# Optimization experiments

Hardware: AMD Instinct MI355X
Metric: run time of the kernel (lower is better)

The kernel has to match this reference:

```python
import jax, jax.numpy as jnp
import numpy as np

E, TOP_K = 8, 2
NEG_SLOPE = 0.01  # nn.LeakyReLU default


def setup_inputs() -> dict:
    key = jax.random.key(0)
    ks = jax.random.split(key, 8)
    B, S, H, F, R = 2, 4096, 2048, 8192, 16
    s_h = 1.0 / np.sqrt(H)
    s_f = 1.0 / np.sqrt(F)
    s_r = 1.0 / np.sqrt(R)
    return {
        "x": jax.random.normal(ks[0], (B, S, H), jnp.float32),
        "gate_w": jax.random.normal(ks[1], (E, H), jnp.float32) * s_h,
        "w1_A": jax.random.normal(ks[2], (E, R, H), jnp.float32) * s_h,
        "w1_B": jax.random.normal(ks[3], (E, F, R), jnp.float32) * s_r,
        "w2_A": jax.random.normal(ks[4], (E, R, F), jnp.float32) * s_f,
        "w2_B": jax.random.normal(ks[5], (E, H, R), jnp.float32) * s_r,
        "w3_A": jax.random.normal(ks[6], (E, R, H), jnp.float32) * s_h,
        "w3_B": jax.random.normal(ks[7], (E, F, R), jnp.float32) * s_r,
    }


def reference(x, gate_w, w1_A, w1_B, w2_A, w2_B, w3_A, w3_B):
    B, S, H = x.shape
    xs = x.reshape(-1, H)  # [T,H]
    # router: softmax in fp32, top-k, renormalize (matches torch code)
    logits = xs @ gate_w.T  # [T,E]
    probs = jax.nn.softmax(logits.astype(jnp.float32), axis=-1)
    rw, sel = jax.lax.top_k(probs, TOP_K)  # [T,K]
    rw = rw / jnp.sum(rw, axis=-1, keepdims=True)
    rw = rw.astype(x.dtype)
    # per-token per-expert combine weight (0 if expert not selected) [T,E]
    w_te = jnp.sum(jax.nn.one_hot(sel, E, dtype=rw.dtype) * rw[..., None], axis=1)
    out = jnp.zeros_like(xs)
    for e in range(E):  # small fixed expert loop; avoids [E,T,F] blowup
        h1 = (xs @ w1_A[e].T) @ w1_B[e].T          # [T,F]
        h3 = (xs @ w3_A[e].T) @ w3_B[e].T          # [T,F]
        h = jnp.where(h1 >= 0, h1, NEG_SLOPE * h1) * h3
        y = (h @ w2_A[e].T) @ w2_B[e].T            # [T,H]
        out = out + y * w_te[:, e:e + 1]
    return out.reshape(B, S, H), rw
```

## Files before the change

kernel.cpp:

```cpp
#include <hip/hip_runtime.h>
#include <hip/hip_bf16.h>

typedef __attribute__((ext_vector_type(8))) short short8;
typedef __attribute__((ext_vector_type(4))) float f32x4;
typedef __hip_bfloat16 bf16;

static constexpr int T_TOK = 8192;
static constexpr int HD    = 2048;
static constexpr int FD    = 8192;
static constexpr int NE    = 8;

#define MFMA16(a,b,c) __builtin_amdgcn_mfma_f32_16x16x32_bf16((a),(b),(c),0,0,0)

__global__ __launch_bounds__(256) void k_convert(
    const float* __restrict__ w1A, const float* __restrict__ w1B,
    const float* __restrict__ w2A, const float* __restrict__ w2B,
    const float* __restrict__ w3A, const float* __restrict__ w3B,
    bf16* __restrict__ bw1a3, bf16* __restrict__ bw1b, bf16* __restrict__ bw3b,
    bf16* __restrict__ bw2apk, bf16* __restrict__ bw2b, int* __restrict__ cnt)
{
  int i = blockIdx.x * 256 + threadIdx.x;
  if (blockIdx.x == 0 && threadIdx.x < 16) cnt[threadIdx.x] = 0;
  bw1b[i] = __float2bfloat16(w1B[i]);
  bw3b[i] = __float2bfloat16(w3B[i]);
  {
    int f = i & (FD - 1); int er = i >> 13; int e = er >> 4; int r = er & 15;
    int ft = f >> 5; int fo = f & 31;
    int sub = fo >> 4; int lg = (fo >> 2) & 3; int j = sub * 4 + (fo & 3);
    int lane = lg * 16 + r;
    bw2apk[((e * 256 + ft) * 64 + lane) * 8 + j] = __float2bfloat16(w2A[i]);
  }
  if (i < 256 * HD) {
    int h = i & (HD - 1); int nn = i >> 11; int e = nn >> 5; int rr = nn & 31;
    float v = (rr < 16) ? w1A[(e * 16 + rr) * HD + h] : w3A[(e * 16 + (rr - 16)) * HD + h];
    bw1a3[e * 65536 + (h >> 5) * 1024 + rr * 32 + (h & 31)] = __float2bfloat16(v);
  }
  if (i < NE * HD * 16) bw2b[i] = __float2bfloat16(w2B[i]);
}

__global__ __launch_bounds__(512) void k_router(
    const float* __restrict__ x, const float* __restrict__ gw,
    float* __restrict__ rw_out, int* __restrict__ cnt,
    int* __restrict__ tok, float* __restrict__ wl, int* __restrict__ selT,
    bf16* __restrict__ bx, int use_bx)
{
  int tid = threadIdx.x;
  int j = tid >> 5;
  int r = tid & 31;
  int t = blockIdx.x * 16 + j;

  const float4* xr = reinterpret_cast<const float4*>(x + (size_t)t * HD);
  float p[8];
#pragma unroll
  for (int e = 0; e < 8; e++) p[e] = 0.f;
#pragma unroll 4
  for (int it = 0; it < 16; it++) {
    float4 xv = xr[it * 32 + r];
#pragma unroll
    for (int e = 0; e < 8; e++) {
      float4 gv = reinterpret_cast<const float4*>(gw + e * HD)[it * 32 + r];
      p[e] += xv.x * gv.x + xv.y * gv.y + xv.z * gv.z + xv.w * gv.w;
    }
    if (use_bx) {
      alignas(8) bf16 tb[4];
      tb[0] = __float2bfloat16(xv.x); tb[1] = __float2bfloat16(xv.y);
      tb[2] = __float2bfloat16(xv.z); tb[3] = __float2bfloat16(xv.w);
      *reinterpret_cast<uint2*>(bx + (size_t)t * HD + (it * 32 + r) * 4) =
          *reinterpret_cast<const uint2*>(tb);
    }
  }
#pragma unroll
  for (int e = 0; e < 8; e++) {
#pragma unroll
    for (int m = 1; m <= 16; m <<= 1) p[e] += __shfl_xor(p[e], m);
  }

  __shared__ int   se0[16], se1[16];
  __shared__ float sw0[16], sw1[16];
  if (r == 0) {
    float m = -1e30f;
#pragma unroll
    for (int e = 0; e < 8; e++) m = fmaxf(m, p[e]);
    float q[8];
#pragma unroll
    for (int e = 0; e < 8; e++) q[e] = __expf(p[e] - m);
    int i0 = 0; float b0 = q[0];
#pragma unroll
    for (int e = 1; e < 8; e++) if (q[e] > b0) { b0 = q[e]; i0 = e; }
    int i1 = -1; float b1 = -1.f;
#pragma unroll
    for (int e = 0; e < 8; e++) if (e != i0 && q[e] > b1) { b1 = q[e]; i1 = e; }
    float inv = 1.f / (b0 + b1);
    float r0 = b0 * inv, r1 = b1 * inv;
    rw_out[t * 2 + 0] = r0; rw_out[t * 2 + 1] = r1;
    selT[t] = i0 | (i1 << 8);
    se0[j] = i0; se1[j] = i1; sw0[j] = r0; sw1[j] = r1;
  }
  __syncthreads();
  if (tid < 16) {
    int ls = tid, e = ls >> 1, slot = ls & 1;
    int c = 0;
#pragma unroll
    for (int jj = 0; jj < 16; jj++)
      c += (slot == 0 ? (se0[jj] == e) : (se1[jj] == e)) ? 1 : 0;
    if (c > 0) {
      int base = atomicAdd(&cnt[ls], c);
      int k = 0;
#pragma unroll
      for (int jj = 0; jj < 16; jj++) {
        bool hit = (slot == 0 ? (se0[jj] == e) : (se1[jj] == e));
        if (hit) {
          tok[ls * T_TOK + base + k] = blockIdx.x * 16 + jj;
          wl [ls * T_TOK + base + k] = (slot == 0 ? sw0[jj] : sw1[jj]);
          k++;
        }
      }
    }
  }
}

#define LDW(FT, B1, B3, W2) { \
    int f0_ = w * 1024 + (FT) * 32; \
    _Pragma("unroll") \
    for (int sub = 0; sub < 2; sub++) { \
      int f_ = f0_ + sub * 16 + lm; \
      B1[sub] = *reinterpret_cast<const short8*>(w1e + f_ * 16 + r8); \
      B3[sub] = *reinterpret_cast<const short8*>(w3e + f_ * 16 + r8); \
    } \
    W2 = *reinterpret_cast<const short8*>(w2e + ((size_t)(f0_ >> 5) * 64 + l) * 8); }

#define CMP(B1, B3, W2) \
  _Pragma("unroll") \
  for (int m = 0; m < 2; m++) { \
    short8 hfrag; \
    _Pragma("unroll") \
    for (int sub = 0; sub < 2; sub++) { \
      f32x4 h1 = MFMA16(B1[sub], A1[m], zf); \
      f32x4 h3 = MFMA16(B3[sub], A3[m], zf); \
      _Pragma("unroll") \
      for (int i = 0; i < 4; i++) { \
        float a = h1[i]; \
        float hv = (a >= 0.f ? a : 0.01f * a) * h3[i]; \
        bf16 hb = __float2bfloat16(hv); \
        hfrag[sub * 4 + i] = *reinterpret_cast<short*>(&hb); \
      } \
    } \
    acc[m] = MFMA16(W2, hfrag, acc[m]); }

__global__ __launch_bounds__(512) void k_fused(
    const float* __restrict__ x, const bf16* __restrict__ bx, int use_bx,
    const bf16* __restrict__ bw1a3,
    const bf16* __restrict__ bw1b, const bf16* __restrict__ bw3b,
    const bf16* __restrict__ bw2apk,
    const int* __restrict__ cnt, const int* __restrict__ tok,
    const float* __restrict__ wl, bf16* __restrict__ accbf)
{
  int item = blockIdx.x;
  int ls = ((item & 7) << 1) | ((item >> 3) & 1);
  int pt = item >> 4;
  int n = cnt[ls]; int p0 = pt * 32;
  if (p0 >= n) return;
  int e = ls >> 1;
  int tid = threadIdx.x;
  int w = tid >> 6, l = tid & 63, lm = l & 15, lg = l >> 4;

  __shared__ int toks[32];
  __shared__ __align__(16) bf16 aT[32 * 40];
  __shared__ __align__(16) char uni[4352 * 4];
  float* part = reinterpret_cast<float*>(uni);
  float* red  = reinterpret_cast<float*>(uni);

  const f32x4 zf = {0.f, 0.f, 0.f, 0.f};
  const short8 ZS = {0, 0, 0, 0, 0, 0, 0, 0};

  if (tid < 32) {
    int pos = p0 + tid; if (pos > n - 1) pos = n - 1;
    toks[tid] = tok[ls * T_TOK + pos];
  }
  __syncthreads();

  {
    int tg = w >> 2, ks = w & 3;
    const bf16* be = bw1a3 + e * 65536 + ks * 16384 + lg * 8;
    f32x4 a0 = zf, a1 = zf, a2 = zf, a3 = zf;
    if (use_bx) {
      const bf16* xp = bx + (size_t)toks[tg * 16 + lm] * HD + ks * 512 + lg * 8;
#pragma unroll 4
      for (int k2 = 0; k2 < 8; k2++) {
        short8 af0 = *reinterpret_cast<const short8*>(xp + (2 * k2) * 32);
        short8 af1 = *reinterpret_cast<const short8*>(xp + (2 * k2 + 1) * 32);
        short8 b00 = *reinterpret_cast<const short8*>(be + (2 * k2) * 1024 + lm * 32);
        short8 b01 = *reinterpret_cast<const short8*>(be + (2 * k2) * 1024 + (lm + 16) * 32);
        short8 b10 = *reinterpret_cast<const short8*>(be + (2 * k2 + 1) * 1024 + lm * 32);
        short8 b11 = *reinterpret_cast<const short8*>(be + (2 * k2 + 1) * 1024 + (lm + 16) * 32);
        a0 = MFMA16(af0, b00, a0);
        a1 = MFMA16(af0, b01, a1);
        a2 = MFMA16(af1, b10, a2);
        a3 = MFMA16(af1, b11, a3);
      }
    } else {
      const float* xp = x + (size_t)toks[tg * 16 + lm] * HD + ks * 512 + lg * 8;
#pragma unroll 4
      for (int kk2 = 0; kk2 < 16; kk2++) {
        float4 v0 = *reinterpret_cast<const float4*>(xp + kk2 * 32);
        float4 v1 = *reinterpret_cast<const float4*>(xp + kk2 * 32 + 4);
        alignas(16) bf16 tmp[8];
        tmp[0] = __float2bfloat16(v0.x); tmp[1] = __float2bfloat16(v0.y);
        tmp[2] = __float2bfloat16(v0.z); tmp[3] = __float2bfloat16(v0.w);
        tmp[4] = __float2bfloat16(v1.x); tmp[5] = __float2bfloat16(v1.y);
        tmp[6] = __float2bfloat16(v1.z); tmp[7] = __float2bfloat16(v1.w);
        short8 af = *reinterpret_cast<const short8*>(tmp);
        short8 b0 = *reinterpret_cast<const short8*>(be + kk2 * 1024 + lm * 32);
        short8 b1 = *reinterpret_cast<const short8*>(be + kk2 * 1024 + (lm + 16) * 32);
        a0 = MFMA16(af, b0, a0);
        a1 = MFMA16(af, b1, a1);
      }
    }
    a0 += a2; a1 += a3;
#pragma unroll
    for (int i = 0; i < 4; i++) {
      int row = tg * 16 + lg * 4 + i;
      part[(ks * 32 + row) * 33 + lm]      = a0[i];
      part[(ks * 32 + row) * 33 + 16 + lm] = a1[i];
    }
  }
  __syncthreads();
  {
    int tokr = tid >> 4, c2 = (tid & 15) * 2;
    float s0 = 0.f, s1 = 0.f;
#pragma unroll
    for (int ks = 0; ks < 4; ks++) {
      s0 += part[(ks * 32 + tokr) * 33 + c2];
      s1 += part[(ks * 32 + tokr) * 33 + c2 + 1];
    }
    aT[tokr * 40 + c2]     = __float2bfloat16(s0);
    aT[tokr * 40 + c2 + 1] = __float2bfloat16(s1);
  }
  __syncthreads();

  short8 A1[2], A3[2];
#pragma unroll
  for (int m = 0; m < 2; m++) {
    if (lg < 2) {
      A1[m] = *reinterpret_cast<const short8*>(&aT[(m * 16 + lm) * 40 + lg * 8]);
      A3[m] = *reinterpret_cast<const short8*>(&aT[(m * 16 + lm) * 40 + 16 + lg * 8]);
    } else { A1[m] = ZS; A3[m] = ZS; }
  }
  f32x4 acc[2];
  acc[0] = zf; acc[1] = zf;
  int r8 = (lg & 1) * 8;
  const bf16* w1e = bw1b   + (size_t)e * FD * 16;
  const bf16* w3e = bw3b   + (size_t)e * FD * 16;
  const bf16* w2e = bw2apk + (size_t)e * 131072;

  short8 b1A[2], b3A[2], w2A_;
  short8 b1B[2], b3B[2], w2B_;
  LDW(0, b1A, b3A, w2A_);
  for (int ft = 0; ft < 32; ft += 2) {
    LDW(ft + 1, b1B, b3B, w2B_);
    CMP(b1A, b3A, w2A_);
    if (ft + 2 < 32) { LDW(ft + 2, b1A, b3A, w2A_); }
    CMP(b1B, b3B, w2B_);
  }
#pragma unroll
  for (int m = 0; m < 2; m++)
#pragma unroll
    for (int i = 0; i < 4; i++)
      red[w * 544 + (m * 16 + lm) * 17 + lg * 4 + i] = acc[m][i];
  __syncthreads();
  {
    int p = tid >> 4, rh = tid & 15;
    int pos = p0 + p;
    if (pos < n) {
      float s = 0.f;
#pragma unroll
      for (int ww = 0; ww < 8; ww++) s += red[ww * 544 + p * 17 + rh];
      float wgt = wl[ls * T_TOK + pos];
      int t = toks[p];
      int sl = ls & 1;
      accbf[((size_t)t * 2 + sl) * 16 + rh] = __float2bfloat16(s * wgt);
    }
  }
}

__global__ __launch_bounds__(256) void k_out(
    const bf16* __restrict__ accbf, const bf16* __restrict__ bw2b,
    const int* __restrict__ selT, float* __restrict__ out)
{
  int tpt = blockIdx.x >> 4;
  int ht  = blockIdx.x & 15;
  int tid = threadIdx.x, w = tid >> 6, l = tid & 63, lm = l & 15, lg = l >> 4;
  int t0 = tpt * 64;
  int tA = t0 + w * 16 + lm;
  int r8 = (lg & 1) * 8;
  int slot = lg >> 1;
  short8 A = *reinterpret_cast<const short8*>(accbf + ((size_t)tA * 2 + slot) * 16 + r8);
  int sel = selT[tA];
  int my_e = (slot == 0) ? (sel & 255) : (sel >> 8);

  const short8 ZS = {0, 0, 0, 0, 0, 0, 0, 0};
  const f32x4 zf = {0.f, 0.f, 0.f, 0.f};
  f32x4 y[2][4];
#pragma unroll
  for (int nt = 0; nt < 2; nt++)
#pragma unroll
    for (int hi = 0; hi < 4; hi++) y[nt][hi] = zf;

#pragma unroll
  for (int e = 0; e < 8; e++) {
    short8 Ae = (my_e == e) ? A : ZS;
    const bf16* wbe = bw2b + (size_t)e * HD * 16;
#pragma unroll
    for (int nt = 0; nt < 2; nt++) {
#pragma unroll
      for (int hi = 0; hi < 4; hi++) {
        int h = ht * 128 + nt * 64 + hi * 16 + lm;
        short8 B = *reinterpret_cast<const short8*>(wbe + h * 16 + r8);
        y[nt][hi] = MFMA16(Ae, B, y[nt][hi]);
      }
    }
  }
#pragma unroll
  for (int nt = 0; nt < 2; nt++)
#pragma unroll
    for (int hi = 0; hi < 4; hi++)
#pragma unroll
      for (int i = 0; i < 4; i++)
        out[(size_t)(t0 + w * 16 + lg * 4 + i) * HD + ht * 128 + nt * 64 + hi * 16 + lm]
            = y[nt][hi][i];
}

extern "C" void kernel_launch(void* const* d_in, const int* in_sizes, int n_in,
                              void* d_out, int out_size, void* d_ws, size_t ws_size,
                              hipStream_t stream)
{
  const float* x   = (const float*)d_in[0];
  const float* gw  = (const float*)d_in[1];
  const float* w1A = (const float*)d_in[2];
  const float* w1B = (const float*)d_in[3];
  const float* w2A = (const float*)d_in[4];
  const float* w2B = (const float*)d_in[5];
  const float* w3A = (const float*)d_in[6];
  const float* w3B = (const float*)d_in[7];
  float* out = (float*)d_out;
  float* rw  = out + (size_t)T_TOK * HD;

  char* ws = (char*)d_ws;
  bf16*  bw1a3  = (bf16*)(ws + 0);
  bf16*  bw1b   = (bf16*)(ws + 1048576);
  bf16*  bw3b   = (bf16*)(ws + 3145728);
  bf16*  bw2apk = (bf16*)(ws + 5242880);
  bf16*  bw2b   = (bf16*)(ws + 7340032);
  bf16*  accbf  = (bf16*)(ws + 16252928);
  int*   cnt    = (int*) (ws + 16777216);
  int*   tok    = (int*) (ws + 16777472);
  float* wl     = (float*)(ws + 17301760);
  int*   selT   = (int*) (ws + 17825792);
  bf16*  bx     = (bf16*)(ws + 18874368);
  int use_bx = (ws_size >= (size_t)18874368 + 33554432) ? 1 : 0;

  k_convert<<<dim3(4096), dim3(256), 0, stream>>>(w1A, w1B, w2A, w2B, w3A, w3B,
                                                  bw1a3, bw1b, bw3b, bw2apk, bw2b, cnt);
  k_router <<<dim3(512),  dim3(512), 0, stream>>>(x, gw, rw, cnt, tok, wl, selT, bx, use_bx);
  k_fused  <<<dim3(4096), dim3(512), 0, stream>>>(x, bx, use_bx, bw1a3, bw1b, bw3b, bw2apk,
                                                  cnt, tok, wl, accbf);
  k_out    <<<dim3(2048), dim3(256), 0, stream>>>(accbf, bw2b, selT, out);
}
```

Measured before the change: 126.2 us.

## Merge weight conversion into router kernel and halve fused tile to 16 tokens

Weight conversion and routing now run in one launch, with blocks past 512 doing conversion, and the counter reset moves to a memset. The fused expert kernel processes 16 tokens per block instead of 32 and launches twice as many blocks. Each warp owns a smaller K slice of the rank-projection step, and the leaky-ReLU uses fmaxf. This removes a launch and raises parallelism for the uneven per-expert token counts, at the cost of reloading every weight tile from memory for half as many tokens.

```diff
diff --git a/kernel.cpp b/kernel.cpp
--- a/kernel.cpp
+++ b/kernel.cpp
@@ -12,42 +12,41 @@
 
 #define MFMA16(a,b,c) __builtin_amdgcn_mfma_f32_16x16x32_bf16((a),(b),(c),0,0,0)
 
-__global__ __launch_bounds__(256) void k_convert(
+__global__ __launch_bounds__(512) void k_prep(
     const float* __restrict__ w1A, const float* __restrict__ w1B,
     const float* __restrict__ w2A, const float* __restrict__ w2B,
     const float* __restrict__ w3A, const float* __restrict__ w3B,
     bf16* __restrict__ bw1a3, bf16* __restrict__ bw1b, bf16* __restrict__ bw3b,
-    bf16* __restrict__ bw2apk, bf16* __restrict__ bw2b, int* __restrict__ cnt)
-{
-  int i = blockIdx.x * 256 + threadIdx.x;
-  if (blockIdx.x == 0 && threadIdx.x < 16) cnt[threadIdx.x] = 0;
-  bw1b[i] = __float2bfloat16(w1B[i]);
-  bw3b[i] = __float2bfloat16(w3B[i]);
-  {
-    int f = i & (FD - 1); int er = i >> 13; int e = er >> 4; int r = er & 15;
-    int ft = f >> 5; int fo = f & 31;
-    int sub = fo >> 4; int lg = (fo >> 2) & 3; int j = sub * 4 + (fo & 3);
-    int lane = lg * 16 + r;
-    bw2apk[((e * 256 + ft) * 64 + lane) * 8 + j] = __float2bfloat16(w2A[i]);
-  }
-  if (i < 256 * HD) {
-    int h = i & (HD - 1); int nn = i >> 11; int e = nn >> 5; int rr = nn & 31;
-    float v = (rr < 16) ? w1A[(e * 16 + rr) * HD + h] : w3A[(e * 16 + (rr - 16)) * HD + h];
-    bw1a3[e * 65536 + (h >> 5) * 1024 + rr * 32 + (h & 31)] = __float2bfloat16(v);
-  }
-  if (i < NE * HD * 16) bw2b[i] = __float2bfloat16(w2B[i]);
-}
-
-__global__ __launch_bounds__(512) void k_router(
+    bf16* __restrict__ bw2apk, bf16* __restrict__ bw2b,
     const float* __restrict__ x, const float* __restrict__ gw,
     float* __restrict__ rw_out, int* __restrict__ cnt,
     int* __restrict__ tok, float* __restrict__ wl, int* __restrict__ selT,
     bf16* __restrict__ bx, int use_bx)
 {
   int tid = threadIdx.x;
+  if (blockIdx.x >= 512) {
+    int i = (blockIdx.x - 512) * 512 + tid;
+    bw1b[i] = __float2bfloat16(w1B[i]);
+    bw3b[i] = __float2bfloat16(w3B[i]);
+    {
+      int f = i & (FD - 1); int er = i >> 13; int e = er >> 4; int r = er & 15;
+      int ft = f >> 5; int fo = f & 31;
+      int sub = fo >> 4; int lg = (fo >> 2) & 3; int j = sub * 4 + (fo & 3);
+      int lane = lg * 16 + r;
+      bw2apk[((e * 256 + ft) * 64 + lane) * 8 + j] = __float2bfloat16(w2A[i]);
+    }
+    if (i < 256 * HD) {
+      int h = i & (HD - 1); int nn = i >> 11; int e = nn >> 5; int rr = nn & 31;
+      float v = (rr < 16) ? w1A[(e * 16 + rr) * HD + h] : w3A[(e * 16 + (rr - 16)) * HD + h];
+      bw1a3[e * 65536 + (h >> 5) * 1024 + rr * 32 + (h & 31)] = __float2bfloat16(v);
+    }
+    if (i < NE * HD * 16) bw2b[i] = __float2bfloat16(w2B[i]);
+    return;
+  }
+  int rb = blockIdx.x;
   int j = tid >> 5;
   int r = tid & 31;
-  int t = blockIdx.x * 16 + j;
+  int t = rb * 16 + j;
 
   const float4* xr = reinterpret_cast<const float4*>(x + (size_t)t * HD);
   float p[8];
@@ -110,7 +109,7 @@
       for (int jj = 0; jj < 16; jj++) {
         bool hit = (slot == 0 ? (se0[jj] == e) : (se1[jj] == e));
         if (hit) {
-          tok[ls * T_TOK + base + k] = blockIdx.x * 16 + jj;
+          tok[ls * T_TOK + base + k] = rb * 16 + jj;
           wl [ls * T_TOK + base + k] = (slot == 0 ? sw0[jj] : sw1[jj]);
           k++;
         }
@@ -129,23 +128,21 @@
     } \
     W2 = *reinterpret_cast<const short8*>(w2e + ((size_t)(f0_ >> 5) * 64 + l) * 8); }
 
-#define CMP(B1, B3, W2) \
-  _Pragma("unroll") \
-  for (int m = 0; m < 2; m++) { \
+#define CMP(B1, B3, W2) { \
     short8 hfrag; \
     _Pragma("unroll") \
     for (int sub = 0; sub < 2; sub++) { \
-      f32x4 h1 = MFMA16(B1[sub], A1[m], zf); \
-      f32x4 h3 = MFMA16(B3[sub], A3[m], zf); \
+      f32x4 h1 = MFMA16(B1[sub], A1, zf); \
+      f32x4 h3 = MFMA16(B3[sub], A3, zf); \
       _Pragma("unroll") \
       for (int i = 0; i < 4; i++) { \
         float a = h1[i]; \
-        float hv = (a >= 0.f ? a : 0.01f * a) * h3[i]; \
+        float hv = fmaxf(a, 0.01f * a) * h3[i]; \
         bf16 hb = __float2bfloat16(hv); \
         hfrag[sub * 4 + i] = *reinterpret_cast<short*>(&hb); \
       } \
     } \
-    acc[m] = MFMA16(W2, hfrag, acc[m]); }
+    acc = MFMA16(W2, hfrag, acc); }
 
 __global__ __launch_bounds__(512) void k_fused(
     const float* __restrict__ x, const bf16* __restrict__ bx, int use_bx,
@@ -158,35 +155,35 @@
   int item = blockIdx.x;
   int ls = ((item & 7) << 1) | ((item >> 3) & 1);
   int pt = item >> 4;
-  int n = cnt[ls]; int p0 = pt * 32;
+  int n = cnt[ls]; int p0 = pt * 16;
   if (p0 >= n) return;
   int e = ls >> 1;
   int tid = threadIdx.x;
   int w = tid >> 6, l = tid & 63, lm = l & 15, lg = l >> 4;
 
-  __shared__ int toks[32];
-  __shared__ __align__(16) bf16 aT[32 * 40];
-  __shared__ __align__(16) char uni[4352 * 4];
+  __shared__ int toks[16];
+  __shared__ __align__(16) bf16 aT[16 * 40];
+  __shared__ __align__(16) char uni[8 * 16 * 33 * 4];
   float* part = reinterpret_cast<float*>(uni);
   float* red  = reinterpret_cast<float*>(uni);
 
   const f32x4 zf = {0.f, 0.f, 0.f, 0.f};
   const short8 ZS = {0, 0, 0, 0, 0, 0, 0, 0};
 
-  if (tid < 32) {
+  if (tid < 16) {
     int pos = p0 + tid; if (pos > n - 1) pos = n - 1;
     toks[tid] = tok[ls * T_TOK + pos];
   }
   __syncthreads();
 
   {
-    int tg = w >> 2, ks = w & 3;
-    const bf16* be = bw1a3 + e * 65536 + ks * 16384 + lg * 8;
+    int ks = w;
+    const bf16* be = bw1a3 + e * 65536 + ks * 8192 + lg * 8;
     f32x4 a0 = zf, a1 = zf, a2 = zf, a3 = zf;
     if (use_bx) {
-      const bf16* xp = bx + (size_t)toks[tg * 16 + lm] * HD + ks * 512 + lg * 8;
-#pragma unroll 4
-      for (int k2 = 0; k2 < 8; k2++) {
+      const bf16* xp = bx + (size_t)toks[lm] * HD + ks * 256 + lg * 8;
+#pragma unroll
+      for (int k2 = 0; k2 < 4; k2++) {
         short8 af0 = *reinterpret_cast<const short8*>(xp + (2 * k2) * 32);
         short8 af1 = *reinterpret_cast<const short8*>(xp + (2 * k2 + 1) * 32);
         short8 b00 = *reinterpret_cast<const short8*>(be + (2 * k2) * 1024 + lm * 32);
@@ -199,9 +196,9 @@
         a3 = MFMA16(af1, b11, a3);
       }
     } else {
-      const float* xp = x + (size_t)toks[tg * 16 + lm] * HD + ks * 512 + lg * 8;
-#pragma unroll 4
-      for (int kk2 = 0; kk2 < 16; kk2++) {
+      const float* xp = x + (size_t)toks[lm] * HD + ks * 256 + lg * 8;
+#pragma unroll
+      for (int kk2 = 0; kk2 < 8; kk2++) {
         float4 v0 = *reinterpret_cast<const float4*>(xp + kk2 * 32);
         float4 v1 = *reinterpret_cast<const float4*>(xp + kk2 * 32 + 4);
         alignas(16) bf16 tmp[8];
@@ -219,35 +216,27 @@
     a0 += a2; a1 += a3;
 #pragma unroll
     for (int i = 0; i < 4; i++) {
-      int row = tg * 16 + lg * 4 + i;
-      part[(ks * 32 + row) * 33 + lm]      = a0[i];
-      part[(ks * 32 + row) * 33 + 16 + lm] = a1[i];
+      int row = lg * 4 + i;
+      part[(w * 16 + row) * 33 + lm]      = a0[i];
+      part[(w * 16 + row) * 33 + 16 + lm] = a1[i];
     }
   }
   __syncthreads();
   {
-    int tokr = tid >> 4, c2 = (tid & 15) * 2;
-    float s0 = 0.f, s1 = 0.f;
-#pragma unroll
-    for (int ks = 0; ks < 4; ks++) {
-      s0 += part[(ks * 32 + tokr) * 33 + c2];
-      s1 += part[(ks * 32 + tokr) * 33 + c2 + 1];
-    }
-    aT[tokr * 40 + c2]     = __float2bfloat16(s0);
-    aT[tokr * 40 + c2 + 1] = __float2bfloat16(s1);
-  }
-  __syncthreads();
-
-  short8 A1[2], A3[2];
-#pragma unroll
-  for (int m = 0; m < 2; m++) {
-    if (lg < 2) {
-      A1[m] = *reinterpret_cast<const short8*>(&aT[(m * 16 + lm) * 40 + lg * 8]);
-      A3[m] = *reinterpret_cast<const short8*>(&aT[(m * 16 + lm) * 40 + 16 + lg * 8]);
-    } else { A1[m] = ZS; A3[m] = ZS; }
-  }
-  f32x4 acc[2];
-  acc[0] = zf; acc[1] = zf;
+    int tokr = tid >> 5, c = tid & 31;
+    float s = 0.f;
+#pragma unroll
+    for (int ks = 0; ks < 8; ks++) s += part[(ks * 16 + tokr) * 33 + c];
+    aT[tokr * 40 + c] = __float2bfloat16(s);
+  }
+  __syncthreads();
+
+  short8 A1, A3;
+  if (lg < 2) {
+    A1 = *reinterpret_cast<const short8*>(&aT[lm * 40 + lg * 8]);
+    A3 = *reinterpret_cast<const short8*>(&aT[lm * 40 + 16 + lg * 8]);
+  } else { A1 = ZS; A3 = ZS; }
+  f32x4 acc = zf;
   int r8 = (lg & 1) * 8;
   const bf16* w1e = bw1b   + (size_t)e * FD * 16;
   const bf16* w3e = bw3b   + (size_t)e * FD * 16;
@@ -263,18 +252,16 @@
     CMP(b1B, b3B, w2B_);
   }
 #pragma unroll
-  for (int m = 0; m < 2; m++)
-#pragma unroll
-    for (int i = 0; i < 4; i++)
-      red[w * 544 + (m * 16 + lm) * 17 + lg * 4 + i] = acc[m][i];
-  __syncthreads();
-  {
+  for (int i = 0; i < 4; i++)
+    red[w * 272 + lm * 17 + lg * 4 + i] = acc[i];
+  __syncthreads();
+  if (tid < 256) {
     int p = tid >> 4, rh = tid & 15;
     int pos = p0 + p;
     if (pos < n) {
       float s = 0.f;
 #pragma unroll
-      for (int ww = 0; ww < 8; ww++) s += red[ww * 544 + p * 17 + rh];
+      for (int ww = 0; ww < 8; ww++) s += red[ww * 272 + p * 17 + rh];
       float wgt = wl[ls * T_TOK + pos];
       int t = toks[p];
       int sl = ls & 1;
@@ -359,10 +346,11 @@
   bf16*  bx     = (bf16*)(ws + 18874368);
   int use_bx = (ws_size >= (size_t)18874368 + 33554432) ? 1 : 0;
 
-  k_convert<<<dim3(4096), dim3(256), 0, stream>>>(w1A, w1B, w2A, w2B, w3A, w3B,
-                                                  bw1a3, bw1b, bw3b, bw2apk, bw2b, cnt);
-  k_router <<<dim3(512),  dim3(512), 0, stream>>>(x, gw, rw, cnt, tok, wl, selT, bx, use_bx);
-  k_fused  <<<dim3(4096), dim3(512), 0, stream>>>(x, bx, use_bx, bw1a3, bw1b, bw3b, bw2apk,
-                                                  cnt, tok, wl, accbf);
-  k_out    <<<dim3(2048), dim3(256), 0, stream>>>(accbf, bw2b, selT, out);
+  hipMemsetAsync(cnt, 0, 64, stream);
+  k_prep <<<dim3(2560), dim3(512), 0, stream>>>(w1A, w1B, w2A, w2B, w3A, w3B,
+                                                bw1a3, bw1b, bw3b, bw2apk, bw2b,
+                                                x, gw, rw, cnt, tok, wl, selT, bx, use_bx);
+  k_fused<<<dim3(8192), dim3(512), 0, stream>>>(x, bx, use_bx, bw1a3, bw1b, bw3b, bw2apk,
+                                                cnt, tok, wl, accbf);
+  k_out  <<<dim3(2048), dim3(256), 0, stream>>>(accbf, bw2b, selT, out);
 }
```

After: 136.9 us. 8.5% more time.

## Split fused expert FFN over two F-halves with fp32 atomic accumulation

Applied to the files above, without the earlier changes.

Splits the F dimension of the fused expert kernel across two blocks per token tile, doubling the grid, so each block walks half the F range. Partial rank-16 results are combined with fp32 atomicAdd into a zeroed buffer instead of a single bf16 store. The output kernel then reads fp32 and converts to bf16. This aims to raise occupancy and parallelism, at the cost of recomputing the token down-projection (x·A) in both halves, adding atomics, and zeroing the buffer.

```diff
diff --git a/kernel.cpp b/kernel.cpp
--- a/kernel.cpp
+++ b/kernel.cpp
@@ -17,10 +17,12 @@
     const float* __restrict__ w2A, const float* __restrict__ w2B,
     const float* __restrict__ w3A, const float* __restrict__ w3B,
     bf16* __restrict__ bw1a3, bf16* __restrict__ bw1b, bf16* __restrict__ bw3b,
-    bf16* __restrict__ bw2apk, bf16* __restrict__ bw2b, int* __restrict__ cnt)
+    bf16* __restrict__ bw2apk, bf16* __restrict__ bw2b, int* __restrict__ cnt,
+    float* __restrict__ accf)
 {
   int i = blockIdx.x * 256 + threadIdx.x;
   if (blockIdx.x == 0 && threadIdx.x < 16) cnt[threadIdx.x] = 0;
+  if (i < T_TOK * 2 * 16) accf[i] = 0.f;
   bw1b[i] = __float2bfloat16(w1B[i]);
   bw3b[i] = __float2bfloat16(w3B[i]);
   {
@@ -120,7 +122,7 @@
 }
 
 #define LDW(FT, B1, B3, W2) { \
-    int f0_ = w * 1024 + (FT) * 32; \
+    int f0_ = fbase + (FT) * 32; \
     _Pragma("unroll") \
     for (int sub = 0; sub < 2; sub++) { \
       int f_ = f0_ + sub * 16 + lm; \
@@ -153,11 +155,12 @@
     const bf16* __restrict__ bw1b, const bf16* __restrict__ bw3b,
     const bf16* __restrict__ bw2apk,
     const int* __restrict__ cnt, const int* __restrict__ tok,
-    const float* __restrict__ wl, bf16* __restrict__ accbf)
+    const float* __restrict__ wl, float* __restrict__ accf)
 {
   int item = blockIdx.x;
   int ls = ((item & 7) << 1) | ((item >> 3) & 1);
-  int pt = item >> 4;
+  int fhalf = (item >> 4) & 1;
+  int pt = item >> 5;
   int n = cnt[ls]; int p0 = pt * 32;
   if (p0 >= n) return;
   int e = ls >> 1;
@@ -249,6 +252,7 @@
   f32x4 acc[2];
   acc[0] = zf; acc[1] = zf;
   int r8 = (lg & 1) * 8;
+  int fbase = fhalf * 4096 + w * 512;
   const bf16* w1e = bw1b   + (size_t)e * FD * 16;
   const bf16* w3e = bw3b   + (size_t)e * FD * 16;
   const bf16* w2e = bw2apk + (size_t)e * 131072;
@@ -256,10 +260,10 @@
   short8 b1A[2], b3A[2], w2A_;
   short8 b1B[2], b3B[2], w2B_;
   LDW(0, b1A, b3A, w2A_);
-  for (int ft = 0; ft < 32; ft += 2) {
+  for (int ft = 0; ft < 16; ft += 2) {
     LDW(ft + 1, b1B, b3B, w2B_);
     CMP(b1A, b3A, w2A_);
-    if (ft + 2 < 32) { LDW(ft + 2, b1A, b3A, w2A_); }
+    if (ft + 2 < 16) { LDW(ft + 2, b1A, b3A, w2A_); }
     CMP(b1B, b3B, w2B_);
   }
 #pragma unroll
@@ -278,13 +282,13 @@
       float wgt = wl[ls * T_TOK + pos];
       int t = toks[p];
       int sl = ls & 1;
-      accbf[((size_t)t * 2 + sl) * 16 + rh] = __float2bfloat16(s * wgt);
+      atomicAdd(&accf[((size_t)t * 2 + sl) * 16 + rh], s * wgt);
     }
   }
 }
 
 __global__ __launch_bounds__(256) void k_out(
-    const bf16* __restrict__ accbf, const bf16* __restrict__ bw2b,
+    const float* __restrict__ accf, const bf16* __restrict__ bw2b,
     const int* __restrict__ selT, float* __restrict__ out)
 {
   int tpt = blockIdx.x >> 4;
@@ -294,7 +298,15 @@
   int tA = t0 + w * 16 + lm;
   int r8 = (lg & 1) * 8;
   int slot = lg >> 1;
-  short8 A = *reinterpret_cast<const short8*>(accbf + ((size_t)tA * 2 + slot) * 16 + r8);
+  const float* ap = accf + ((size_t)tA * 2 + slot) * 16 + r8;
+  float4 av0 = *reinterpret_cast<const float4*>(ap);
+  float4 av1 = *reinterpret_cast<const float4*>(ap + 4);
+  alignas(16) bf16 atmp[8];
+  atmp[0] = __float2bfloat16(av0.x); atmp[1] = __float2bfloat16(av0.y);
+  atmp[2] = __float2bfloat16(av0.z); atmp[3] = __float2bfloat16(av0.w);
+  atmp[4] = __float2bfloat16(av1.x); atmp[5] = __float2bfloat16(av1.y);
+  atmp[6] = __float2bfloat16(av1.z); atmp[7] = __float2bfloat16(av1.w);
+  short8 A = *reinterpret_cast<const short8*>(atmp);
   int sel = selT[tA];
   int my_e = (slot == 0) ? (sel & 255) : (sel >> 8);
 
@@ -351,7 +363,7 @@
   bf16*  bw3b   = (bf16*)(ws + 3145728);
   bf16*  bw2apk = (bf16*)(ws + 5242880);
   bf16*  bw2b   = (bf16*)(ws + 7340032);
-  bf16*  accbf  = (bf16*)(ws + 16252928);
+  float* accf   = (float*)(ws + 8388608);
   int*   cnt    = (int*) (ws + 16777216);
   int*   tok    = (int*) (ws + 16777472);
   float* wl     = (float*)(ws + 17301760);
@@ -360,9 +372,9 @@
   int use_bx = (ws_size >= (size_t)18874368 + 33554432) ? 1 : 0;
 
   k_convert<<<dim3(4096), dim3(256), 0, stream>>>(w1A, w1B, w2A, w2B, w3A, w3B,
-                                                  bw1a3, bw1b, bw3b, bw2apk, bw2b, cnt);
+                                                  bw1a3, bw1b, bw3b, bw2apk, bw2b, cnt, accf);
   k_router <<<dim3(512),  dim3(512), 0, stream>>>(x, gw, rw, cnt, tok, wl, selT, bx, use_bx);
-  k_fused  <<<dim3(4096), dim3(512), 0, stream>>>(x, bx, use_bx, bw1a3, bw1b, bw3b, bw2apk,
-                                                  cnt, tok, wl, accbf);
-  k_out    <<<dim3(2048), dim3(256), 0, stream>>>(accbf, bw2b, selT, out);
-}
+  k_fused  <<<dim3(8192), dim3(512), 0, stream>>>(x, bx, use_bx, bw1a3, bw1b, bw3b, bw2apk,
+                                                  cnt, tok, wl, accf);
+  k_out    <<<dim3(2048), dim3(256), 0, stream>>>(accf, bw2b, selT, out);
+}
```

After: 134.5 us. 6.6% more time.
